# Performance work log

Measured on AMD Instinct MI355X. Metric: run time of the kernel, lower is better.

## Reference

```python
import jax, jax.numpy as jnp
import numpy as np

HIDDEN = 1024


def setup_inputs() -> dict:
    key = jax.random.key(0)
    ks = jax.random.split(key, 8)
    B, S, H = 64, 2048, HIDDEN
    scale = 1.0 / np.sqrt(H)
    return {
        "decoder_hidden": jax.random.normal(ks[0], (B, H), jnp.float32),
        "encoder_outputs": jax.random.normal(ks[1], (B, S, 2 * H), jnp.float32),
        "coverage": jax.random.uniform(ks[2], (B, S), jnp.float32),
        "mask": jnp.ones((B, S), jnp.int32),
        # parameters (nn.Linear weight layout: (out, in); we store transposed for x @ W)
        "W_h": jax.random.normal(ks[3], (2 * H, H), jnp.float32) * scale,
        "W_d": jax.random.normal(ks[4], (H, H), jnp.float32) * scale,
        "W_c": jax.random.normal(ks[5], (1, H), jnp.float32) * scale,
        "v": jax.random.normal(ks[6], (H, 1), jnp.float32) * scale,
    }


def reference(decoder_hidden, encoder_outputs, coverage, mask, W_h, W_d, W_c, v):
    # energy: (B, S, H) = tanh(enc@W_h + dec@W_d broadcast over S + coverage*W_c)
    enc_proj = jnp.einsum("bse,eh->bsh", encoder_outputs, W_h)
    dec_proj = (decoder_hidden @ W_d)[:, None, :]            # (B,1,H)
    cov_proj = coverage[:, :, None] * W_c[0][None, None, :]  # (B,S,H)
    energy = jnp.tanh(enc_proj + dec_proj + cov_proj)
    scores = jnp.einsum("bsh,h->bs", energy, v[:, 0])        # (B,S)
    scores = jnp.where(mask == 0, jnp.float32(-10000.0), scores)
    attn_weights = jax.nn.softmax(scores, axis=1)            # (B,S)
    coverage_new = coverage + attn_weights
    context = jnp.einsum("bs,bse->be", attn_weights, encoder_outputs)  # (B,2H)
    return (context, attn_weights, coverage_new)
```

## Files before the change

### kernel.cpp

```cpp
#include <hip/hip_runtime.h>
#include <hip/hip_bf16.h>
#include <stdint.h>

#define BATCH 64
#define SEQ   2048
#define HID   1024
#define EDIM  2048

#define BM 64
#define BK 32
#define KSTEPS (EDIM / BK)
#define SMEM_BYTES 141568

typedef __bf16 bf16x8 __attribute__((ext_vector_type(8)));
typedef float  f32x16 __attribute__((ext_vector_type(16)));

__device__ __forceinline__ unsigned short f2bf(float x) {
    __hip_bfloat16 h = __float2bfloat16(x);
    return __builtin_bit_cast(unsigned short, h);
}

__device__ __forceinline__ uint4 pack8(float4 f0, float4 f1) {
    uint4 r;
    r.x = (unsigned)f2bf(f0.x) | ((unsigned)f2bf(f0.y) << 16);
    r.y = (unsigned)f2bf(f0.z) | ((unsigned)f2bf(f0.w) << 16);
    r.z = (unsigned)f2bf(f1.x) | ((unsigned)f2bf(f1.y) << 16);
    r.w = (unsigned)f2bf(f1.z) | ((unsigned)f2bf(f1.w) << 16);
    return r;
}

__device__ __forceinline__ void gload16(const void* g, void* l) {
    __builtin_amdgcn_global_load_lds(
        (const __attribute__((address_space(1))) void*)g,
        (__attribute__((address_space(3))) void*)l, 16, 0, 0);
}

__device__ __forceinline__ int a_addr(int row, int g) {
    return ((row << 6) + (g << 4)) ^ ((row & 7) << 4);
}

__global__ void wh_transpose_kernel(const float* __restrict__ Wh,
                                    unsigned short* __restrict__ Wt) {
    __shared__ float tile[32][33];
    int bx = blockIdx.x & 63;
    int by = blockIdx.x >> 6;
    int e0 = bx * 32, h0 = by * 32;
    int tx = threadIdx.x & 31, ty = threadIdx.x >> 5;
    #pragma unroll
    for (int i = 0; i < 4; ++i)
        tile[ty + 8 * i][tx] = Wh[(size_t)(e0 + ty + 8 * i) * HID + h0 + tx];
    __syncthreads();
    if (ty < 4) {
        uint4 wv;
        unsigned short* ws = (unsigned short*)&wv;
        #pragma unroll
        for (int j = 0; j < 8; ++j) ws[j] = f2bf(tile[ty * 8 + j][tx]);
        *(uint4*)&Wt[((size_t)(e0 >> 3) + ty) * 8192 + (size_t)(h0 + tx) * 8] = wv;
    }
}

__global__ void dec_proj_kernel(const float* __restrict__ dec,
                                const float* __restrict__ Wd,
                                float* __restrict__ dp) {
    int gid = blockIdx.x * 256 + threadIdx.x;
    int b = gid >> 10, h = gid & 1023;
    const float* dr = dec + b * HID;
    float acc = 0.f;
    #pragma unroll 4
    for (int k = 0; k < HID; ++k) acc = fmaf(dr[k], Wd[(size_t)k * HID + h], acc);
    dp[gid] = acc;
}

__global__ __launch_bounds__(512, 2) void scores_kernel(
    const float* __restrict__ enc, const float* __restrict__ cov,
    const unsigned short* __restrict__ Wt, const float* __restrict__ dp,
    const float* __restrict__ Wc, const float* __restrict__ vv,
    float* __restrict__ scores)
{
    extern __shared__ char smem[];
    unsigned short* BlS  = (unsigned short*)smem;
    char*  AlB   = smem + 131072;
    float* cov_s = (float*)(smem + 139264);
    float* sred  = (float*)(smem + 139520);

    const int tid  = threadIdx.x;
    const int lane = tid & 63;
    const int wid  = tid >> 6;
    const int l31  = lane & 31;
    const int hi   = lane >> 5;

    const int b  = blockIdx.x >> 5;
    const int s0 = (blockIdx.x & 31) * BM;

    const float* Abase = enc + (size_t)(b * SEQ + s0) * EDIM;

    const int arow = tid >> 2;
    const int ag   = tid & 3;

    f32x16 acc[2][4];
    #pragma unroll
    for (int mi = 0; mi < 2; ++mi)
        #pragma unroll
        for (int nj = 0; nj < 4; ++nj)
            #pragma unroll
            for (int r = 0; r < 16; ++r) acc[mi][nj][r] = 0.f;

    if (tid < BM) cov_s[tid] = cov[b * SEQ + s0 + tid];

    {
        const unsigned short* bsrc = Wt + (size_t)tid * 8;
        unsigned short* bdst = BlS + tid * 8;
        #pragma unroll
        for (int j = 0; j < 8; ++j)
            gload16(bsrc + (size_t)j * 4096, bdst + j * 4096);
        if (tid < 256) {
            const float* ap = Abase + (size_t)arow * EDIM + ag * 8;
            *(uint4*)(AlB + a_addr(arow, ag)) =
                pack8(*(const float4*)ap, *(const float4*)(ap + 4));
        }
    }
    __syncthreads();

    float4 a0n, a1n;
    for (int kk = 0; kk < KSTEPS; ++kk) {
        const int cur = kk & 1, nxt = cur ^ 1;
        const unsigned short* Bcur = BlS + cur * 32768;
        const char* Acur = AlB + cur * 4096;

        if (kk + 1 < KSTEPS) {
            const unsigned short* bsrc = Wt + (size_t)(kk + 1) * 32768 + (size_t)tid * 8;
            unsigned short* bdst = BlS + nxt * 32768 + tid * 8;
            #pragma unroll
            for (int j = 0; j < 8; ++j)
                gload16(bsrc + (size_t)j * 4096, bdst + j * 4096);
            if (tid < 256) {
                const float* ap = Abase + (size_t)arow * EDIM + (kk + 1) * BK + ag * 8;
                a0n = *(const float4*)ap;
                a1n = *(const float4*)(ap + 4);
            }
        }

        #pragma unroll
        for (int ks = 0; ks < 2; ++ks) {
            const int g = 2 * ks + hi;
            bf16x8 afr0 = *(const bf16x8*)(Acur + a_addr(l31, g));
            bf16x8 afr1 = *(const bf16x8*)(Acur + a_addr(32 + l31, g));
            #pragma unroll
            for (int nj = 0; nj < 4; ++nj) {
                bf16x8 bfr = *(const bf16x8*)(Bcur +
                    ((size_t)g * 8192 + (size_t)(wid * 128 + nj * 32 + l31) * 8));
                acc[0][nj] = __builtin_amdgcn_mfma_f32_32x32x16_bf16(
                    afr0, bfr, acc[0][nj], 0, 0, 0);
                acc[1][nj] = __builtin_amdgcn_mfma_f32_32x32x16_bf16(
                    afr1, bfr, acc[1][nj], 0, 0, 0);
            }
        }

        if (kk + 1 < KSTEPS && tid < 256)
            *(uint4*)(AlB + nxt * 4096 + a_addr(arow, ag)) = pack8(a0n, a1n);
        __syncthreads();
    }

    float dv[4], wcv[4], vvv[4];
    #pragma unroll
    for (int nj = 0; nj < 4; ++nj) {
        const int h = wid * 128 + nj * 32 + l31;
        dv[nj]  = dp[b * HID + h];
        wcv[nj] = Wc[h];
        vvv[nj] = vv[h];
    }
    #pragma unroll
    for (int mi = 0; mi < 2; ++mi) {
        #pragma unroll
        for (int r = 0; r < 16; ++r) {
            const int row = mi * 32 + (r & 3) + 8 * (r >> 2) + 4 * hi;
            const float cv = cov_s[row];
            float x = 0.f;
            #pragma unroll
            for (int nj = 0; nj < 4; ++nj) {
                float pre = acc[mi][nj][r] + dv[nj] + cv * wcv[nj];
                float pc = fminf(pre, 20.0f);
                float e2 = __expf(2.0f * pc);
                x = fmaf((e2 - 1.0f) / (e2 + 1.0f), vvv[nj], x);
            }
            x += __shfl_xor(x, 1);
            x += __shfl_xor(x, 2);
            x += __shfl_xor(x, 4);
            x += __shfl_xor(x, 8);
            x += __shfl_xor(x, 16);
            if (l31 == 0) sred[row * 8 + wid] = x;
        }
    }
    __syncthreads();
    if (tid < BM) {
        float s = 0.f;
        #pragma unroll
        for (int w = 0; w < 8; ++w) s += sred[tid * 8 + w];
        scores[b * SEQ + s0 + tid] = s;
    }
}

__global__ void softmax_kernel(const float* __restrict__ scores,
                               const int* __restrict__ mask,
                               const float* __restrict__ cov,
                               float* __restrict__ out)
{
    __shared__ float red[8];
    int b = blockIdx.x, tid = threadIdx.x;
    float vals[8];
    float mx = -1e30f;
    #pragma unroll
    for (int i = 0; i < 8; ++i) {
        int s = tid + i * 256;
        float sc = scores[b * SEQ + s];
        sc = (mask[b * SEQ + s] == 0) ? -10000.0f : sc;
        vals[i] = sc;
        mx = fmaxf(mx, sc);
    }
    for (int m = 1; m < 64; m <<= 1) mx = fmaxf(mx, __shfl_xor(mx, m));
    if ((tid & 63) == 0) red[tid >> 6] = mx;
    __syncthreads();
    mx = fmaxf(fmaxf(red[0], red[1]), fmaxf(red[2], red[3]));
    float sum = 0.f;
    #pragma unroll
    for (int i = 0; i < 8; ++i) { vals[i] = __expf(vals[i] - mx); sum += vals[i]; }
    for (int m = 1; m < 64; m <<= 1) sum += __shfl_xor(sum, m);
    if ((tid & 63) == 0) red[4 + (tid >> 6)] = sum;
    __syncthreads();
    sum = red[4] + red[5] + red[6] + red[7];
    float inv = 1.0f / sum;
    float* attn = out + BATCH * EDIM;
    float* covn = attn + BATCH * SEQ;
    #pragma unroll
    for (int i = 0; i < 8; ++i) {
        int s = tid + i * 256;
        float w = vals[i] * inv;
        attn[b * SEQ + s] = w;
        covn[b * SEQ + s] = cov[b * SEQ + s] + w;
    }
}

__global__ void context_kernel(const float* __restrict__ enc,
                               const float* __restrict__ attn,
                               float* __restrict__ ctx)
{
    __shared__ float w_s[SEQ];
    int b  = blockIdx.x >> 3;
    int e0 = (blockIdx.x & 7) * 256;
    int tid = threadIdx.x;
    for (int i = tid; i < SEQ; i += 256) w_s[i] = attn[b * SEQ + i];
    __syncthreads();
    const float* ep = enc + (size_t)b * SEQ * EDIM + e0 + tid;
    float acc = 0.f;
    #pragma unroll 8
    for (int s = 0; s < SEQ; ++s) acc = fmaf(w_s[s], ep[(size_t)s * EDIM], acc);
    ctx[b * EDIM + e0 + tid] = acc;
}

extern "C" void kernel_launch(void* const* d_in, const int* in_sizes, int n_in,
                              void* d_out, int out_size, void* d_ws, size_t ws_size,
                              hipStream_t stream) {
    const float* dec  = (const float*)d_in[0];
    const float* enc  = (const float*)d_in[1];
    const float* cov  = (const float*)d_in[2];
    const int*   mask = (const int*)d_in[3];
    const float* Wh   = (const float*)d_in[4];
    const float* Wd   = (const float*)d_in[5];
    const float* Wc   = (const float*)d_in[6];
    const float* v    = (const float*)d_in[7];
    float* out = (float*)d_out;

    unsigned short* Wt = (unsigned short*)d_ws;
    float* dp     = (float*)((char*)d_ws + (size_t)HID * EDIM * 2);
    float* scores = dp + BATCH * HID;

    (void)hipFuncSetAttribute((const void*)scores_kernel,
                              hipFuncAttributeMaxDynamicSharedMemorySize, SMEM_BYTES);

    wh_transpose_kernel<<<dim3(64 * 32), dim3(256), 0, stream>>>(Wh, Wt);
    dec_proj_kernel<<<dim3(BATCH * HID / 256), dim3(256), 0, stream>>>(dec, Wd, dp);
    scores_kernel<<<dim3(BATCH * (SEQ / BM)), dim3(512), SMEM_BYTES, stream>>>(
        enc, cov, Wt, dp, Wc, v, scores);
    softmax_kernel<<<dim3(BATCH), dim3(256), 0, stream>>>(scores, mask, cov, out);
    context_kernel<<<dim3(BATCH * (EDIM / 256)), dim3(256), 0, stream>>>(enc, out + BATCH * EDIM, out);
}
```

Measured before the change: 1.159 ms.

## Retile scores GEMM to 128x512 tiles with split-N halves and partial-score sum

The scores GEMM tile changes from 64 rows x full 1024 hidden to 128 rows x 512 hidden. Each block handles one half of the hidden dimension, and the two partial scores are summed in the softmax kernel. The Wt layout is rearranged to match, and the block index mapping pairs halves so they share encoder rows in cache. This halves per-block LDS so more blocks can be resident, and uses all 512 threads for A loads. The cost is that encoder rows are read and converted twice, once per half. Encoder loads in the GEMM and the context kernel also switch to nontemporal loads.

After: 1.141 ms. Within noise of the previous version (-1.6%).

```diff
diff --git a/kernel.cpp b/kernel.cpp
--- a/kernel.cpp
+++ b/kernel.cpp
@@ -7,20 +7,22 @@
 #define HID   1024
 #define EDIM  2048
 
-#define BM 64
+#define BM 128
+#define BN 512
 #define BK 32
 #define KSTEPS (EDIM / BK)
-#define SMEM_BYTES 141568
+#define SMEM_BYTES (65536 + 16384 + 512 + 2048)
 
 typedef __bf16 bf16x8 __attribute__((ext_vector_type(8)));
 typedef float  f32x16 __attribute__((ext_vector_type(16)));
+typedef float  f32x4v __attribute__((ext_vector_type(4)));
 
 __device__ __forceinline__ unsigned short f2bf(float x) {
     __hip_bfloat16 h = __float2bfloat16(x);
     return __builtin_bit_cast(unsigned short, h);
 }
 
-__device__ __forceinline__ uint4 pack8(float4 f0, float4 f1) {
+__device__ __forceinline__ uint4 pack8(f32x4v f0, f32x4v f1) {
     uint4 r;
     r.x = (unsigned)f2bf(f0.x) | ((unsigned)f2bf(f0.y) << 16);
     r.y = (unsigned)f2bf(f0.z) | ((unsigned)f2bf(f0.w) << 16);
@@ -33,6 +35,10 @@
     __builtin_amdgcn_global_load_lds(
         (const __attribute__((address_space(1))) void*)g,
         (__attribute__((address_space(3))) void*)l, 16, 0, 0);
+}
+
+__device__ __forceinline__ f32x4v ntload4(const float* p) {
+    return __builtin_nontemporal_load((const f32x4v*)p);
 }
 
 __device__ __forceinline__ int a_addr(int row, int g) {
@@ -55,7 +61,8 @@
         unsigned short* ws = (unsigned short*)&wv;
         #pragma unroll
         for (int j = 0; j < 8; ++j) ws[j] = f2bf(tile[ty * 8 + j][tx]);
-        *(uint4*)&Wt[((size_t)(e0 >> 3) + ty) * 8192 + (size_t)(h0 + tx) * 8] = wv;
+        int h = h0 + tx;
+        *(uint4*)&Wt[(size_t)((e0 >> 3) + ty) * 8192 + (h >> 9) * 4096 + (h & 511) * 8] = wv;
     }
 }
 
@@ -75,22 +82,27 @@
     const float* __restrict__ enc, const float* __restrict__ cov,
     const unsigned short* __restrict__ Wt, const float* __restrict__ dp,
     const float* __restrict__ Wc, const float* __restrict__ vv,
-    float* __restrict__ scores)
+    float* __restrict__ spart_out)
 {
     extern __shared__ char smem[];
     unsigned short* BlS  = (unsigned short*)smem;
-    char*  AlB   = smem + 131072;
-    float* cov_s = (float*)(smem + 139264);
-    float* sred  = (float*)(smem + 139520);
+    char*  AlB   = smem + 65536;
+    float* cov_s = (float*)(smem + 81920);
+    float* sred  = (float*)(smem + 82432);
 
     const int tid  = threadIdx.x;
     const int lane = tid & 63;
     const int wid  = tid >> 6;
+    const int wm   = wid >> 2;
+    const int wn   = wid & 3;
     const int l31  = lane & 31;
     const int hi   = lane >> 5;
 
-    const int b  = blockIdx.x >> 5;
-    const int s0 = (blockIdx.x & 31) * BM;
+    const int bid  = blockIdx.x;
+    const int half = (bid & 7) >> 2;
+    const int m    = ((bid >> 3) << 2) | (bid & 3);
+    const int b    = m >> 4;
+    const int s0   = (m & 15) * BM;
 
     const float* Abase = enc + (size_t)(b * SEQ + s0) * EDIM;
 
@@ -108,47 +120,43 @@
     if (tid < BM) cov_s[tid] = cov[b * SEQ + s0 + tid];
 
     {
-        const unsigned short* bsrc = Wt + (size_t)tid * 8;
+        const unsigned short* bsrc = Wt + half * 4096 + (size_t)tid * 8;
         unsigned short* bdst = BlS + tid * 8;
         #pragma unroll
-        for (int j = 0; j < 8; ++j)
-            gload16(bsrc + (size_t)j * 4096, bdst + j * 4096);
-        if (tid < 256) {
-            const float* ap = Abase + (size_t)arow * EDIM + ag * 8;
-            *(uint4*)(AlB + a_addr(arow, ag)) =
-                pack8(*(const float4*)ap, *(const float4*)(ap + 4));
-        }
-    }
-    __syncthreads();
-
-    float4 a0n, a1n;
+        for (int j = 0; j < 4; ++j)
+            gload16(bsrc + (size_t)j * 8192, bdst + j * 4096);
+        const float* ap = Abase + (size_t)arow * EDIM + ag * 8;
+        *(uint4*)(AlB + a_addr(arow, ag)) = pack8(ntload4(ap), ntload4(ap + 4));
+    }
+    __syncthreads();
+
+    f32x4v a0n, a1n;
     for (int kk = 0; kk < KSTEPS; ++kk) {
         const int cur = kk & 1, nxt = cur ^ 1;
-        const unsigned short* Bcur = BlS + cur * 32768;
-        const char* Acur = AlB + cur * 4096;
+        const unsigned short* Bcur = BlS + cur * 16384;
+        const char* Acur = AlB + cur * 8192;
 
         if (kk + 1 < KSTEPS) {
-            const unsigned short* bsrc = Wt + (size_t)(kk + 1) * 32768 + (size_t)tid * 8;
-            unsigned short* bdst = BlS + nxt * 32768 + tid * 8;
-            #pragma unroll
-            for (int j = 0; j < 8; ++j)
-                gload16(bsrc + (size_t)j * 4096, bdst + j * 4096);
-            if (tid < 256) {
-                const float* ap = Abase + (size_t)arow * EDIM + (kk + 1) * BK + ag * 8;
-                a0n = *(const float4*)ap;
-                a1n = *(const float4*)(ap + 4);
-            }
+            const unsigned short* bsrc =
+                Wt + (size_t)(kk + 1) * 32768 + half * 4096 + (size_t)tid * 8;
+            unsigned short* bdst = BlS + nxt * 16384 + tid * 8;
+            #pragma unroll
+            for (int j = 0; j < 4; ++j)
+                gload16(bsrc + (size_t)j * 8192, bdst + j * 4096);
+            const float* ap = Abase + (size_t)arow * EDIM + (kk + 1) * BK + ag * 8;
+            a0n = ntload4(ap);
+            a1n = ntload4(ap + 4);
         }
 
         #pragma unroll
         for (int ks = 0; ks < 2; ++ks) {
             const int g = 2 * ks + hi;
-            bf16x8 afr0 = *(const bf16x8*)(Acur + a_addr(l31, g));
-            bf16x8 afr1 = *(const bf16x8*)(Acur + a_addr(32 + l31, g));
+            bf16x8 afr0 = *(const bf16x8*)(Acur + a_addr(wm * 64 + l31, g));
+            bf16x8 afr1 = *(const bf16x8*)(Acur + a_addr(wm * 64 + 32 + l31, g));
             #pragma unroll
             for (int nj = 0; nj < 4; ++nj) {
                 bf16x8 bfr = *(const bf16x8*)(Bcur +
-                    ((size_t)g * 8192 + (size_t)(wid * 128 + nj * 32 + l31) * 8));
+                    (size_t)g * 4096 + (size_t)(wn * 128 + nj * 32 + l31) * 8);
                 acc[0][nj] = __builtin_amdgcn_mfma_f32_32x32x16_bf16(
                     afr0, bfr, acc[0][nj], 0, 0, 0);
                 acc[1][nj] = __builtin_amdgcn_mfma_f32_32x32x16_bf16(
@@ -156,15 +164,15 @@
             }
         }
 
-        if (kk + 1 < KSTEPS && tid < 256)
-            *(uint4*)(AlB + nxt * 4096 + a_addr(arow, ag)) = pack8(a0n, a1n);
+        if (kk + 1 < KSTEPS)
+            *(uint4*)(AlB + nxt * 8192 + a_addr(arow, ag)) = pack8(a0n, a1n);
         __syncthreads();
     }
 
     float dv[4], wcv[4], vvv[4];
     #pragma unroll
     for (int nj = 0; nj < 4; ++nj) {
-        const int h = wid * 128 + nj * 32 + l31;
+        const int h = half * BN + wn * 128 + nj * 32 + l31;
         dv[nj]  = dp[b * HID + h];
         wcv[nj] = Wc[h];
         vvv[nj] = vv[h];
@@ -173,7 +181,7 @@
     for (int mi = 0; mi < 2; ++mi) {
         #pragma unroll
         for (int r = 0; r < 16; ++r) {
-            const int row = mi * 32 + (r & 3) + 8 * (r >> 2) + 4 * hi;
+            const int row = wm * 64 + mi * 32 + (r & 3) + 8 * (r >> 2) + 4 * hi;
             const float cv = cov_s[row];
             float x = 0.f;
             #pragma unroll
@@ -188,19 +196,17 @@
             x += __shfl_xor(x, 4);
             x += __shfl_xor(x, 8);
             x += __shfl_xor(x, 16);
-            if (l31 == 0) sred[row * 8 + wid] = x;
+            if (l31 == 0) sred[row * 4 + wn] = x;
         }
     }
     __syncthreads();
     if (tid < BM) {
-        float s = 0.f;
-        #pragma unroll
-        for (int w = 0; w < 8; ++w) s += sred[tid * 8 + w];
-        scores[b * SEQ + s0 + tid] = s;
-    }
-}
-
-__global__ void softmax_kernel(const float* __restrict__ scores,
+        float s = sred[tid * 4] + sred[tid * 4 + 1] + sred[tid * 4 + 2] + sred[tid * 4 + 3];
+        spart_out[(size_t)half * BATCH * SEQ + b * SEQ + s0 + tid] = s;
+    }
+}
+
+__global__ void softmax_kernel(const float* __restrict__ spart,
                                const int* __restrict__ mask,
                                const float* __restrict__ cov,
                                float* __restrict__ out)
@@ -212,7 +218,7 @@
     #pragma unroll
     for (int i = 0; i < 8; ++i) {
         int s = tid + i * 256;
-        float sc = scores[b * SEQ + s];
+        float sc = spart[b * SEQ + s] + spart[BATCH * SEQ + b * SEQ + s];
         sc = (mask[b * SEQ + s] == 0) ? -10000.0f : sc;
         vals[i] = sc;
         mx = fmaxf(mx, sc);
@@ -253,7 +259,8 @@
     const float* ep = enc + (size_t)b * SEQ * EDIM + e0 + tid;
     float acc = 0.f;
     #pragma unroll 8
-    for (int s = 0; s < SEQ; ++s) acc = fmaf(w_s[s], ep[(size_t)s * EDIM], acc);
+    for (int s = 0; s < SEQ; ++s)
+        acc = fmaf(w_s[s], __builtin_nontemporal_load(ep + (size_t)s * EDIM), acc);
     ctx[b * EDIM + e0 + tid] = acc;
 }
 
@@ -271,16 +278,16 @@
     float* out = (float*)d_out;
 
     unsigned short* Wt = (unsigned short*)d_ws;
-    float* dp     = (float*)((char*)d_ws + (size_t)HID * EDIM * 2);
-    float* scores = dp + BATCH * HID;
+    float* dp    = (float*)((char*)d_ws + (size_t)HID * EDIM * 2);
+    float* spart = dp + BATCH * HID;
 
     (void)hipFuncSetAttribute((const void*)scores_kernel,
                               hipFuncAttributeMaxDynamicSharedMemorySize, SMEM_BYTES);
 
     wh_transpose_kernel<<<dim3(64 * 32), dim3(256), 0, stream>>>(Wh, Wt);
     dec_proj_kernel<<<dim3(BATCH * HID / 256), dim3(256), 0, stream>>>(dec, Wd, dp);
-    scores_kernel<<<dim3(BATCH * (SEQ / BM)), dim3(512), SMEM_BYTES, stream>>>(
-        enc, cov, Wt, dp, Wc, v, scores);
-    softmax_kernel<<<dim3(BATCH), dim3(256), 0, stream>>>(scores, mask, cov, out);
+    scores_kernel<<<dim3((SEQ * BATCH / BM) * 2), dim3(512), SMEM_BYTES, stream>>>(
+        enc, cov, Wt, dp, Wc, v, spart);
+    softmax_kernel<<<dim3(BATCH), dim3(256), 0, stream>>>(spart, mask, cov, out);
     context_kernel<<<dim3(BATCH * (EDIM / 256)), dim3(256), 0, stream>>>(enc, out + BATCH * EDIM, out);
 }
```
